# Kernel optimization log

Measured on AMD Instinct MI355X. Metric: run time of the kernel, lower is better.

## Reference

```python
import jax, jax.numpy as jnp
import numpy as np

# ---- grid / solver constants (from opt) ----
NZ, NX = 300, 400
NPML, NPAD = 32, 0
NZP = NZ + 2 * NPML + NPAD   # 364 padded depth
NXP = NX + 2 * NPML          # 464 padded width
NSTEPS = 200
NSHOTS = 2
DX = 0.01    # km (moduli scaled by 1e-6 => velocities in km/s)
DT = 0.001   # s
SRC_Z = NPML + 2
REC_Z = NPML + 2


def _pad_model(m):
    # edge-replicate into the CPML halo + bottom pad, as ft.padding does
    return jnp.pad(m, ((NPML, NPML + NPAD), (NPML, NPML)), mode='edge')


def _sponge():
    # smooth absorbing profile in the nPml halo (sponge approximation of CPML)
    i = np.arange(NZP, dtype=np.float32)
    j = np.arange(NXP, dtype=np.float32)
    dz = np.clip(np.maximum(NPML - i, i - (NZP - 1 - NPML - NPAD)), 0, NPML) / NPML
    dx_ = np.clip(np.maximum(NPML - j, j - (NXP - 1 - NPML)), 0, NPML) / NPML
    d = dz[:, None] ** 2 + dx_[None, :] ** 2
    return jnp.asarray(np.exp(-0.1 * d), dtype=jnp.float32)


# staggered-grid finite differences (zero outside the grid)
def _dxf(f):
    return (jnp.pad(f[:, 1:], ((0, 0), (0, 1))) - f) / DX

def _dxb(f):
    return (f - jnp.pad(f[:, :-1], ((0, 0), (1, 0)))) / DX

def _dzf(f):
    return (jnp.pad(f[1:, :], ((0, 1), (0, 0))) - f) / DX

def _dzb(f):
    return (f - jnp.pad(f[:-1, :], ((1, 0), (0, 0)))) / DX


def _propagate(lam, mu, rho, stf, src_x, damp):
    """Elastic velocity-stress FDTD for one shot. stf: [NSTEPS]. Returns recs [NSTEPS, NX]."""
    lam2mu = lam + 2.0 * mu
    dt_rho = DT / rho
    zero = jnp.zeros((NZP, NXP), jnp.float32)

    def step(carry, s):
        vx, vz, sxx, szz, sxz = carry
        vx = (vx + dt_rho * (_dxf(sxx) + _dzb(sxz))) * damp
        vz = (vz + dt_rho * (_dxb(sxz) + _dzf(szz))) * damp
        dvx_dx = _dxb(vx)
        dvz_dz = _dzb(vz)
        sxx = (sxx + DT * (lam2mu * dvx_dx + lam * dvz_dz)) * damp
        szz = (szz + DT * (lam * dvx_dx + lam2mu * dvz_dz)) * damp
        sxz = (sxz + DT * mu * (_dzf(vx) + _dxf(vz))) * damp
        # explosive source injected into normal stresses
        sxx = sxx.at[SRC_Z, src_x].add(s * DT)
        szz = szz.at[SRC_Z, src_x].add(s * DT)
        rec = vx[REC_Z, NPML:NPML + NX]  # surface receiver line
        return (vx, vz, sxx, szz, sxz), rec

    init = (zero, zero, zero, zero, zero)
    _, recs = jax.lax.scan(step, init, stf)
    return recs


def _forward(Vp, Vs, Den, Stf, Mask, Shot_ids):
    Vp_pad = _pad_model(Vp)
    Vs_pad = _pad_model(Vs)
    Den_pad = _pad_model(Den)
    # masked models: gradient flows only where Mask == 1
    Vp_m = Mask * Vp_pad + (1.0 - Mask) * jax.lax.stop_gradient(Vp_pad)
    Vs_m = Mask * Vs_pad + (1.0 - Mask) * jax.lax.stop_gradient(Vs_pad)
    Den_m = Mask * Den_pad + (1.0 - Mask) * jax.lax.stop_gradient(Den_pad)
    Lam = (Vp_m ** 2 - 2.0 * Vs_m ** 2) * Den_m / 1.0e6
    Mu = Vs_m ** 2 * Den_m / 1.0e6

    damp = _sponge()
    ids = Shot_ids.astype(jnp.int32)
    src_x = NPML + 20 + ids * ((NX - 40) // NSHOTS)  # per-shot source x position
    stf = Stf[ids]                                   # [nshots, NSTEPS]
    recs = jax.vmap(lambda s, sx: _propagate(Lam, Mu, Den_m, s, sx, damp))(stf, src_x)
    return 0.5 * jnp.sum(recs.astype(jnp.float32) ** 2)  # scalar misfit


def setup_inputs() -> dict:
    key = jax.random.key(0)
    k1, k2 = jax.random.split(key)
    Vp = 2000.0 + 1500.0 * jax.random.uniform(k1, (NZ, NX), jnp.float32)   # m/s
    Vs = Vp / 1.732
    Den = 2000.0 + 500.0 * jax.random.uniform(k2, (NZ, NX), jnp.float32)   # kg/m^3
    # Ricker wavelet source, f0 = 10 Hz, shared across shots
    t = jnp.arange(NSTEPS, dtype=jnp.float32) * DT - 0.1
    f0 = 10.0
    arg = (jnp.pi * f0 * t) ** 2
    ricker = (1.0 - 2.0 * arg) * jnp.exp(-arg)
    Stf = jnp.broadcast_to(ricker, (NSHOTS, NSTEPS)).astype(jnp.float32)
    Mask = jnp.ones((NZP, NXP), jnp.float32)
    Shot_ids = jnp.arange(NSHOTS, dtype=jnp.int32)
    return {"Vp": Vp, "Vs": Vs, "Den": Den, "Stf": Stf, "Mask": Mask,
            "Shot_ids": Shot_ids, "ngpu": 1}


def reference(Vp, Vs, Den, Stf, Mask, Shot_ids, ngpu):
    return _forward(Vp, Vs, Den, Stf, Mask, Shot_ids)
```

## Files before the change

kernel.cpp:

```cpp
#include <hip/hip_runtime.h>
#include <cmath>

typedef unsigned long long u64;

namespace {
constexpr int kNZ = 300, kNX = 400;
constexpr int kNPML = 32;
constexpr int kNZP = 364, kNXP = 464;
constexpr int kNSTEPS = 200, kNSHOTS = 2;
constexpr int kSRC_Z = 34, kREC_Z = 34;
constexpr float kDT = 0.001f;
constexpr float kINV_DX = 100.0f;

constexpr int kR = 4;
constexpr int kNSLAB = 92;
constexpr int kNB = kNSLAB - 1;
constexpr int kBlocks = kNSHOTS * kNSLAB;
constexpr int kThreads = 512;
constexpr int kPitch = 468;
constexpr int kFStride = kR * kPitch;

constexpr int kFlagStride = 32;
constexpr int kHaloBase = 16384;
constexpr int kHaloCount = 2 * kNSHOTS * kNB * 2 * 6 * kNXP;
constexpr int kPartOff = kHaloBase + kHaloCount;
}

#define ALD(p)    __hip_atomic_load((p),       __ATOMIC_RELAXED, __HIP_MEMORY_SCOPE_AGENT)
#define AST(p, v) __hip_atomic_store((p), (v), __ATOMIC_RELAXED, __HIP_MEMORY_SCOPE_AGENT)

#define STRESS_ROW(r, VZU, VXD)                                                \
  {                                                                            \
    const float vxC = fvx[r], vzC = fvz[r];                                    \
    const float vxL = Lvx[(r) * kPitch + lc - 1];                              \
    const float vzR = Lvz[(r) * kPitch + lc + 1];                              \
    const float dvx = vxC - vxL;                                               \
    const float dvz = vzC - (VZU);                                             \
    float nsxx = (fsxx[r] + (rl2m[r] * dvx + rlam[r] * dvz)) * rdamp[r];       \
    float nszz = (fszz[r] + (rlam[r] * dvx + rl2m[r] * dvz)) * rdamp[r];       \
    float nsxz = (fsxz[r] + rmu[r] * (((VXD) - vxC) + (vzR - vzC))) * rdamp[r];\
    if ((r) == rsrc) { nsxx += srcm * sval; nszz += srcm * sval; }             \
    fsxx[r] = nsxx; fszz[r] = nszz; fsxz[r] = nsxz;                            \
    Lsxx[(r) * kPitch + lc] = nsxx;                                            \
    Lsxz[(r) * kPitch + lc] = nsxz;                                            \
  }

__global__ __launch_bounds__(kThreads, 1) void fwi_sim_kernel(
    const float* __restrict__ Vp, const float* __restrict__ Vs,
    const float* __restrict__ Den, const float* __restrict__ Stf,
    const int* __restrict__ Shot_ids, float* __restrict__ ws,
    float* __restrict__ out) {
    __shared__ float L[4 * kFStride];
    float* Lvx  = L;
    float* Lvz  = L + kFStride;
    float* Lsxx = L + 2 * kFStride;
    float* Lsxz = L + 3 * kFStride;

    const int blk  = blockIdx.x;
    const int s    = blk / kNSLAB;
    const int slab = blk - s * kNSLAB;
    const int r0   = slab * kR;
    const int tid  = threadIdx.x;
    const bool active = tid < kNXP;
    const int lc = tid + 1;

    int*   flags = (int*)ws;
    float* halo  = ws + kHaloBase;
    u64*   part  = (u64*)(ws + kPartOff);

    for (int q = tid; q < 4 * kFStride; q += kThreads) L[q] = 0.0f;

    auto modAt = [&](int i, int j, float& dtr_, float& dmp_, float& lam_,
                     float& mu_, float& l2m_) {
        dtr_ = dmp_ = lam_ = mu_ = l2m_ = 0.0f;
        if (i >= 0 && i < kNZP && j >= 0 && j < kNXP) {
            int iz = i - kNPML; iz = iz < 0 ? 0 : (iz > kNZ - 1 ? kNZ - 1 : iz);
            int jx = j - kNPML; jx = jx < 0 ? 0 : (jx > kNX - 1 ? kNX - 1 : jx);
            const float vp  = Vp[iz * kNX + jx];
            const float vs  = Vs[iz * kNX + jx];
            const float rho = Den[iz * kNX + jx];
            const float m = vs * vs * rho * 1e-6f;
            const float l = (vp * vp - 2.0f * vs * vs) * rho * 1e-6f;
            const float sc = kDT * kINV_DX;
            float dz = fmaxf((float)(kNPML - i), (float)(i - (kNZP - 1 - kNPML)));
            dz = fminf(fmaxf(dz, 0.0f), (float)kNPML) * (1.0f / kNPML);
            float dxx = fmaxf((float)(kNPML - j), (float)(j - (kNXP - 1 - kNPML)));
            dxx = fminf(fmaxf(dxx, 0.0f), (float)kNPML) * (1.0f / kNPML);
            dmp_ = expf(-0.1f * (dz * dz + dxx * dxx));
            dtr_ = kDT / rho * kINV_DX;
            lam_ = l * sc;
            mu_  = m * sc;
            l2m_ = (l + 2.0f * m) * sc;
        }
    };
    float rdtr[kR], rdamp[kR], rlam[kR], rmu[kR], rl2m[kR];
    float dtrT = 0, dmpT = 0, dtrB = 0, dmpB = 0;
    if (active) {
#pragma unroll
        for (int r = 0; r < kR; ++r)
            modAt(r0 + r, tid, rdtr[r], rdamp[r], rlam[r], rmu[r], rl2m[r]);
        float d0, d1, d2;
        modAt(r0 - 1, tid, dtrT, dmpT, d0, d1, d2);
        modAt(r0 + kR, tid, dtrB, dmpB, d0, d1, d2);
    }

    const int id  = Shot_ids[s];
    const int sxp = kNPML + 20 + id * ((kNX - 40) / kNSHOTS);
    const float* stf = Stf + id * kNSTEPS;
    const int rsrc = kSRC_Z - r0;
    const int rrec = kREC_Z - r0;
    const bool isRecBlock = (rrec >= 0 && rrec < kR);
    const float srcm = (active && tid == sxp) ? 1.0f : 0.0f;
    const float recm = (active && (unsigned)(tid - kNPML) < (unsigned)kNX) ? 1.0f : 0.0f;

    const bool hasTop = (slab > 0);
    const bool hasBot = (slab < kNSLAB - 1);
    int* ftopw = hasTop ? &flags[((s * kNB + (slab - 1)) * 2 + 1) * kFlagStride] : nullptr;
    int* fbotw = hasBot ? &flags[((s * kNB + slab) * 2 + 0) * kFlagStride] : nullptr;
    int* ftopr = hasTop ? &flags[((s * kNB + (slab - 1)) * 2 + 0) * kFlagStride] : nullptr;
    int* fbotr = hasBot ? &flags[((s * kNB + slab) * 2 + 1) * kFlagStride] : nullptr;
    auto hbase = [&](int buf, int b, int dir) {
        return halo + ((((buf * kNSHOTS + s) * kNB + b) * 2 + dir) * 6) * kNXP;
    };

    float fvx[kR]  = {}, fvz[kR]  = {}, fsxx[kR] = {}, fszz[kR] = {}, fsxz[kR] = {};
    float rsum = 0.0f;
    __syncthreads();

    for (int t = 0; t < kNSTEPS; ++t) {
        const int rb = (t & 1) ^ 1;
        const int wb = t & 1;

        if (active) {
#pragma unroll
            for (int r = 1; r <= kR - 2; ++r) {
                const float sxxC = fsxx[r];
                const float sxzC = fsxz[r];
                const float szzC = fszz[r];
                const float sxxR = Lsxx[r * kPitch + lc + 1];
                const float sxzL = Lsxz[r * kPitch + lc - 1];
                const float nvx = (fvx[r] + rdtr[r] * ((sxxR - sxxC) + (sxzC - fsxz[r - 1]))) * rdamp[r];
                const float nvz = (fvz[r] + rdtr[r] * ((sxzC - sxzL) + (fszz[r + 1] - szzC))) * rdamp[r];
                fvx[r] = nvx;
                fvz[r] = nvz;
                Lvx[r * kPitch + lc] = nvx;
                Lvz[r * kPitch + lc] = nvz;
                if (r == rrec) rsum += recm * nvx * nvx;
            }
        }

        if (t > 0) {
            if (hasTop & hasBot) {
                for (;;) {
                    const int a = ALD(ftopr);
                    const int b = ALD(fbotr);
                    if (a >= t && b >= t) break;
                }
            } else if (hasTop) {
                while (ALD(ftopr) < t) {}
            } else if (hasBot) {
                while (ALD(fbotr) < t) {}
            }
        }

        float h_vxT = 0, h_vzT = 0, h_sxxT = 0, h_szzT = 0, h_sxzT = 0, h_sxz2T = 0;
        float h_sxxT_r = 0, h_sxzT_l = 0;
        float h_vxB = 0, h_vzB = 0, h_sxxB = 0, h_sxzB = 0, h_szzB = 0, h_szz2B = 0;
        float h_sxxB_r = 0, h_sxzB_l = 0;
        if (t > 0 && active && hasTop) {
            const float* hb = hbase(rb, slab - 1, 0);
            h_vxT   = ALD(hb + tid);
            h_vzT   = ALD(hb + kNXP + tid);
            h_sxxT  = ALD(hb + 2 * kNXP + tid);
            h_szzT  = ALD(hb + 3 * kNXP + tid);
            h_sxzT  = ALD(hb + 4 * kNXP + tid);
            h_sxz2T = ALD(hb + 5 * kNXP + tid);
            if (tid < kNXP - 1) h_sxxT_r = ALD(hb + 2 * kNXP + tid + 1);
            if (tid > 0)        h_sxzT_l = ALD(hb + 4 * kNXP + tid - 1);
        }
        if (t > 0 && active && hasBot) {
            const float* hb = hbase(rb, slab, 1);
            h_vxB   = ALD(hb + tid);
            h_vzB   = ALD(hb + kNXP + tid);
            h_sxxB  = ALD(hb + 2 * kNXP + tid);
            h_sxzB  = ALD(hb + 3 * kNXP + tid);
            h_szzB  = ALD(hb + 4 * kNXP + tid);
            h_szz2B = ALD(hb + 5 * kNXP + tid);
            if (tid < kNXP - 1) h_sxxB_r = ALD(hb + 2 * kNXP + tid + 1);
            if (tid > 0)        h_sxzB_l = ALD(hb + 3 * kNXP + tid - 1);
        }

        float nvxT = 0, nvzT = 0, nvxB = 0, nvzB = 0;
        if (active) {
            nvxT = (h_vxT + dtrT * ((h_sxxT_r - h_sxxT) + (h_sxzT - h_sxz2T))) * dmpT;
            nvzT = (h_vzT + dtrT * ((h_sxzT - h_sxzT_l) + (fszz[0] - h_szzT))) * dmpT;
            nvxB = (h_vxB + dtrB * ((h_sxxB_r - h_sxxB) + (h_sxzB - fsxz[kR - 1]))) * dmpB;
            nvzB = (h_vzB + dtrB * ((h_sxzB - h_sxzB_l) + (h_szz2B - h_szzB))) * dmpB;
            {
                const float sxxC = fsxx[0], sxzC = fsxz[0], szzC = fszz[0];
                const float sxxR = Lsxx[lc + 1];
                const float sxzL = Lsxz[lc - 1];
                const float nvx = (fvx[0] + rdtr[0] * ((sxxR - sxxC) + (sxzC - h_sxzT))) * rdamp[0];
                const float nvz = (fvz[0] + rdtr[0] * ((sxzC - sxzL) + (fszz[1] - szzC))) * rdamp[0];
                fvx[0] = nvx; fvz[0] = nvz;
                Lvx[lc] = nvx; Lvz[lc] = nvz;
                if (0 == rrec) rsum += recm * nvx * nvx;
            }
            {
                const int r = kR - 1;
                const float sxxC = fsxx[r], sxzC = fsxz[r], szzC = fszz[r];
                const float sxxR = Lsxx[r * kPitch + lc + 1];
                const float sxzL = Lsxz[r * kPitch + lc - 1];
                const float nvx = (fvx[r] + rdtr[r] * ((sxxR - sxxC) + (sxzC - fsxz[r - 1]))) * rdamp[r];
                const float nvz = (fvz[r] + rdtr[r] * ((sxzC - sxzL) + (h_szzB - szzC))) * rdamp[r];
                fvx[r] = nvx; fvz[r] = nvz;
                Lvx[r * kPitch + lc] = nvx; Lvz[r * kPitch + lc] = nvz;
                if (r == rrec) rsum += recm * nvx * nvx;
            }
        }
        __syncthreads();

        if (active) {
            const float sval = stf[t] * kDT;
            STRESS_ROW(0, nvzT, fvx[1])
            STRESS_ROW(1, fvz[0], fvx[2])
            if (hasTop) {
                float* hb = hbase(wb, slab - 1, 1);
                AST(hb + tid,            fvx[0]);
                AST(hb + kNXP + tid,     fvz[0]);
                AST(hb + 2 * kNXP + tid, fsxx[0]);
                AST(hb + 3 * kNXP + tid, fsxz[0]);
                AST(hb + 4 * kNXP + tid, fszz[0]);
                AST(hb + 5 * kNXP + tid, fszz[1]);
            }
            STRESS_ROW(3, fvz[2], nvxB)
            STRESS_ROW(2, fvz[1], fvx[3])
            if (hasBot) {
                float* hb = hbase(wb, slab, 0);
                AST(hb + tid,            fvx[kR - 1]);
                AST(hb + kNXP + tid,     fvz[kR - 1]);
                AST(hb + 2 * kNXP + tid, fsxx[kR - 1]);
                AST(hb + 3 * kNXP + tid, fszz[kR - 1]);
                AST(hb + 4 * kNXP + tid, fsxz[kR - 1]);
                AST(hb + 5 * kNXP + tid, fsxz[kR - 2]);
            }
        }
        __syncthreads();
        if (tid == 0 && hasTop) AST(ftopw, t + 1);
        if (tid == 1 && hasBot) AST(fbotw, t + 1);
    }

    for (int off = 32; off > 0; off >>= 1) rsum += __shfl_down(rsum, off, 64);
    __syncthreads();
    if ((tid & 63) == 0) L[tid >> 6] = rsum;
    __syncthreads();
    if (isRecBlock && tid == 0) {
        float tot = 0.0f;
#pragma unroll
        for (int w = 0; w < kThreads / 64; ++w) tot += L[w];
        const u64 word = ((u64)1 << 32) | (u64)__float_as_uint(tot);
        AST(&part[s], word);
    }
    if (blk == 0 && tid == 0) {
        u64 v0, v1;
        do { v0 = ALD(&part[0]); } while ((int)(v0 >> 32) < 1);
        do { v1 = ALD(&part[1]); } while ((int)(v1 >> 32) < 1);
        out[0] = 0.5f * (__uint_as_float((unsigned)v0) + __uint_as_float((unsigned)v1));
    }
}

extern "C" void kernel_launch(void* const* d_in, const int* in_sizes, int n_in,
                              void* d_out, int out_size, void* d_ws, size_t ws_size,
                              hipStream_t stream) {
    const float* Vp  = (const float*)d_in[0];
    const float* Vs  = (const float*)d_in[1];
    const float* Den = (const float*)d_in[2];
    const float* Stf = (const float*)d_in[3];
    const int* Shot_ids = (const int*)d_in[5];
    float* out = (float*)d_out;
    float* ws  = (float*)d_ws;

    fwi_sim_kernel<<<kBlocks, kThreads, 0, stream>>>(Vp, Vs, Den, Stf,
                                                     Shot_ids, ws, out);
}
```

Measured before the change: 635.6 us.

## Use per-wave neighbor flags and lighter barriers in slab halo exchange

Each wave now publishes its own completion flag after its halo stores drain with s_waitcnt vmcnt(0). This replaces the block-wide __syncthreads followed by a single flag store. Consumers prefetch all eight per-wave flags of each neighbor before the interior velocity update and spin on their minimum. __syncthreads is replaced with an inline-asm lgkmcnt wait plus s_barrier, and the stress rows are folded into one unrolled loop. The aim is to cut barrier cost and hide flag-poll latency behind compute, at the cost of more atomic loads and fragile hand-written memory ordering.

After: 752.1 us. 1.18x slower.

```diff
diff --git a/kernel.cpp b/kernel.cpp
--- a/kernel.cpp
+++ b/kernel.cpp
@@ -17,6 +17,7 @@
 constexpr int kNB = kNSLAB - 1;
 constexpr int kBlocks = kNSHOTS * kNSLAB;
 constexpr int kThreads = 512;
+constexpr int kWaves = kThreads / 64;
 constexpr int kPitch = 468;
 constexpr int kFStride = kR * kPitch;
 
@@ -28,22 +29,9 @@
 
 #define ALD(p)    __hip_atomic_load((p),       __ATOMIC_RELAXED, __HIP_MEMORY_SCOPE_AGENT)
 #define AST(p, v) __hip_atomic_store((p), (v), __ATOMIC_RELAXED, __HIP_MEMORY_SCOPE_AGENT)
-
-#define STRESS_ROW(r, VZU, VXD)                                                \
-  {                                                                            \
-    const float vxC = fvx[r], vzC = fvz[r];                                    \
-    const float vxL = Lvx[(r) * kPitch + lc - 1];                              \
-    const float vzR = Lvz[(r) * kPitch + lc + 1];                              \
-    const float dvx = vxC - vxL;                                               \
-    const float dvz = vzC - (VZU);                                             \
-    float nsxx = (fsxx[r] + (rl2m[r] * dvx + rlam[r] * dvz)) * rdamp[r];       \
-    float nszz = (fszz[r] + (rlam[r] * dvx + rl2m[r] * dvz)) * rdamp[r];       \
-    float nsxz = (fsxz[r] + rmu[r] * (((VXD) - vxC) + (vzR - vzC))) * rdamp[r];\
-    if ((r) == rsrc) { nsxx += srcm * sval; nszz += srcm * sval; }             \
-    fsxx[r] = nsxx; fszz[r] = nszz; fsxz[r] = nsxz;                            \
-    Lsxx[(r) * kPitch + lc] = nsxx;                                            \
-    Lsxz[(r) * kPitch + lc] = nsxz;                                            \
-  }
+#define LDS_BAR() asm volatile("s_waitcnt lgkmcnt(0)\n\ts_barrier" ::: "memory")
+
+__device__ __forceinline__ int imn(int a, int b) { return a < b ? a : b; }
 
 __global__ __launch_bounds__(kThreads, 1) void fwi_sim_kernel(
     const float* __restrict__ Vp, const float* __restrict__ Vs,
@@ -63,6 +51,8 @@
     const int tid  = threadIdx.x;
     const bool active = tid < kNXP;
     const int lc = tid + 1;
+    const int lane = tid & 63;
+    const int wv   = tid >> 6;
 
     int*   flags = (int*)ws;
     float* halo  = ws + kHaloBase;
@@ -131,6 +121,18 @@
         const int rb = (t & 1) ^ 1;
         const int wb = t & 1;
 
+        int ft[kWaves], fb[kWaves];
+        if (t > 0) {
+            if (hasTop) {
+#pragma unroll
+                for (int w = 0; w < kWaves; ++w) ft[w] = ALD(ftopr + w);
+            }
+            if (hasBot) {
+#pragma unroll
+                for (int w = 0; w < kWaves; ++w) fb[w] = ALD(fbotr + w);
+            }
+        }
+
         if (active) {
 #pragma unroll
             for (int r = 1; r <= kR - 2; ++r) {
@@ -150,16 +152,25 @@
         }
 
         if (t > 0) {
-            if (hasTop & hasBot) {
-                for (;;) {
-                    const int a = ALD(ftopr);
-                    const int b = ALD(fbotr);
-                    if (a >= t && b >= t) break;
+            int m = 0x7fffffff;
+            if (hasTop) {
+#pragma unroll
+                for (int w = 0; w < kWaves; ++w) m = imn(m, ft[w]);
+            }
+            if (hasBot) {
+#pragma unroll
+                for (int w = 0; w < kWaves; ++w) m = imn(m, fb[w]);
+            }
+            while (m < t) {
+                m = 0x7fffffff;
+                if (hasTop) {
+#pragma unroll
+                    for (int w = 0; w < kWaves; ++w) m = imn(m, ALD(ftopr + w));
                 }
-            } else if (hasTop) {
-                while (ALD(ftopr) < t) {}
-            } else if (hasBot) {
-                while (ALD(fbotr) < t) {}
+                if (hasBot) {
+#pragma unroll
+                    for (int w = 0; w < kWaves; ++w) m = imn(m, ALD(fbotr + w));
+                }
             }
         }
 
@@ -218,12 +229,30 @@
                 if (r == rrec) rsum += recm * nvx * nvx;
             }
         }
-        __syncthreads();
+        LDS_BAR();
 
         if (active) {
             const float sval = stf[t] * kDT;
-            STRESS_ROW(0, nvzT, fvx[1])
-            STRESS_ROW(1, fvz[0], fvx[2])
+#pragma unroll
+            for (int r = 0; r < kR; ++r) {
+                const float vxC = fvx[r];
+                const float vzC = fvz[r];
+                const float vxL = Lvx[r * kPitch + lc - 1];
+                const float vzR = Lvz[r * kPitch + lc + 1];
+                const float vzU = (r > 0) ? fvz[r - 1] : nvzT;
+                const float vxD = (r < kR - 1) ? fvx[r + 1] : nvxB;
+                const float dvx = vxC - vxL;
+                const float dvz = vzC - vzU;
+                float nsxx = (fsxx[r] + (rl2m[r] * dvx + rlam[r] * dvz)) * rdamp[r];
+                float nszz = (fszz[r] + (rlam[r] * dvx + rl2m[r] * dvz)) * rdamp[r];
+                float nsxz = (fsxz[r] + rmu[r] * ((vxD - vxC) + (vzR - vzC))) * rdamp[r];
+                if (r == rsrc) { nsxx += srcm * sval; nszz += srcm * sval; }
+                fsxx[r] = nsxx;
+                fszz[r] = nszz;
+                fsxz[r] = nsxz;
+                Lsxx[r * kPitch + lc] = nsxx;
+                Lsxz[r * kPitch + lc] = nsxz;
+            }
             if (hasTop) {
                 float* hb = hbase(wb, slab - 1, 1);
                 AST(hb + tid,            fvx[0]);
@@ -233,8 +262,6 @@
                 AST(hb + 4 * kNXP + tid, fszz[0]);
                 AST(hb + 5 * kNXP + tid, fszz[1]);
             }
-            STRESS_ROW(3, fvz[2], nvxB)
-            STRESS_ROW(2, fvz[1], fvx[3])
             if (hasBot) {
                 float* hb = hbase(wb, slab, 0);
                 AST(hb + tid,            fvx[kR - 1]);
@@ -245,9 +272,11 @@
                 AST(hb + 5 * kNXP + tid, fsxz[kR - 2]);
             }
         }
-        __syncthreads();
-        if (tid == 0 && hasTop) AST(ftopw, t + 1);
-        if (tid == 1 && hasBot) AST(fbotw, t + 1);
+
+        asm volatile("s_waitcnt vmcnt(0)" ::: "memory");
+        if (lane == 0 && hasTop) AST(ftopw + wv, t + 1);
+        if (lane == 1 && hasBot) AST(fbotw + wv, t + 1);
+        LDS_BAR();
     }
 
     for (int off = 32; off > 0; off >>= 1) rsum += __shfl_down(rsum, off, 64);
```
